# Kernel tuning notes

Measured on AMD Instinct MI355X. Metric: run time of the kernel, lower is better.

Reference implementation:

```python
import jax, jax.numpy as jnp
import numpy as np
import math

B, L, C, D, H, NLAYERS, DFF = 256, 100, 55, 512, 8, 3, 64


def _pos_embedding(length, d_model):
    pos = np.arange(length, dtype=np.float32)[:, None]
    div = np.exp(np.arange(0, d_model, 2, dtype=np.float32) * (-math.log(10000.0) / d_model))
    pe = np.zeros((length, d_model), dtype=np.float32)
    pe[:, 0::2] = np.sin(pos * div)
    pe[:, 1::2] = np.cos(pos * div)
    return jnp.asarray(pe)


def setup_inputs() -> dict:
    key = jax.random.key(0)
    ks = jax.random.split(key, 12)
    r = lambda k, s, sc: jax.random.normal(k, s, dtype=jnp.float32) * sc
    sD = 1.0 / math.sqrt(D)
    return {
        'x': r(ks[0], (B, L, C), 1.0),
        'tok_w': r(ks[1], (D, C, 3), 1.0 / math.sqrt(3 * C)),  # Conv1d(c_in->d_model, k=3, circular, no bias)
        'pe': _pos_embedding(L, D),
        'Wq': r(ks[2], (NLAYERS, D, D), sD), 'bq': jnp.zeros((NLAYERS, D), jnp.float32),
        'Wk': r(ks[3], (NLAYERS, D, D), sD), 'bk': jnp.zeros((NLAYERS, D), jnp.float32),
        'Wv': r(ks[4], (NLAYERS, D, D), sD), 'bv': jnp.zeros((NLAYERS, D), jnp.float32),
        'Wsig': r(ks[5], (NLAYERS, H, D), sD), 'bsig': jnp.zeros((NLAYERS, H), jnp.float32),
        'Wo': r(ks[6], (NLAYERS, D, D), sD), 'bo': jnp.zeros((NLAYERS, D), jnp.float32),
        'W1': r(ks[7], (NLAYERS, DFF, D), sD), 'b1': jnp.zeros((NLAYERS, DFF), jnp.float32),  # conv1 (1x1)
        'W2': r(ks[8], (NLAYERS, D, DFF), 1.0 / math.sqrt(DFF)), 'b2': jnp.zeros((NLAYERS, D), jnp.float32),  # conv2 (1x1)
        'proj_w': r(ks[9], (C, D), sD), 'proj_b': jnp.zeros((C,), jnp.float32),
    }


def _forward(x, tok_w, pe, Wq, bq, Wk, bk, Wv, bv, Wsig, bsig, Wo, bo, W1, b1, W2, b2, proj_w, proj_b):
    Bx, Lx, _ = x.shape
    nlayers, nH = Wsig.shape[0], Wsig.shape[1]
    d_model = Wq.shape[1]
    dk = d_model // nH
    scale = 1.0 / math.sqrt(dk)
    # token embedding: circular-padded Conv1d(k=3, no bias), then + positional embedding
    xc = jnp.pad(jnp.swapaxes(x, 1, 2), ((0, 0), (0, 0), (1, 1)), mode='wrap')  # [B,C,L+2]
    emb = jax.lax.conv_general_dilated(xc, tok_w, (1,), 'VALID', dimension_numbers=('NCW', 'OIW', 'NCW'))
    h = jnp.swapaxes(emb, 1, 2) + pe[None]  # [B,L,D]
    dist = jnp.abs(jnp.arange(Lx)[:, None] - jnp.arange(Lx)[None, :]).astype(h.dtype)  # |i-j|
    for l in range(nlayers):
        q = h @ Wq[l].T + bq[l]                       # [B,L,D]
        k = (h @ Wk[l].T + bk[l]).reshape(Bx, Lx, nH, dk)
        v = (h @ Wv[l].T + bv[l]).reshape(Bx, Lx, nH, dk)
        # NOTE: source applies sigma projection to the *projected* queries
        sigma = q @ Wsig[l].T + bsig[l]               # [B,L,H]
        qh = q.reshape(Bx, Lx, nH, dk)
        scores = jnp.einsum('blhe,bshe->bhls', qh, k)  # [B,H,L,L]
        series = jax.nn.softmax(scale * scores, axis=-1)
        # Gaussian prior branch (mask_flag=False; computed in source forward,
        # does not feed the module's returned output)
        sg = jnp.swapaxes(sigma, 1, 2)                 # [B,H,L]
        sg = jnp.power(3.0, jax.nn.sigmoid(sg * 5.0) + 1e-5) - 1.0
        sgE = sg[..., None]                            # [B,H,L,1]
        _prior = jnp.exp(-(dist ** 2)[None, None] / (2.0 * sgE ** 2)) / (math.sqrt(2.0 * math.pi) * sgE)
        o = jnp.einsum('bhls,bshd->blhd', series, v).reshape(Bx, Lx, d_model)
        h = h + (o @ Wo[l].T + bo[l])                  # residual 1 (dropout=identity at eval)
        y = jax.nn.gelu(h @ W1[l].T + b1[l], approximate=False)  # conv1 1x1 + gelu
        h = h + (y @ W2[l].T + b2[l])                  # conv2 1x1, residual 2
    return h @ proj_w.T + proj_b                       # [B,L,c_out]


def reference(x, tok_w, pe, Wq, bq, Wk, bk, Wv, bv, Wsig, bsig, Wo, bo, W1, b1, W2, b2, proj_w, proj_b):
    return _forward(x, tok_w, pe, Wq, bq, Wk, bk, Wv, bv, Wsig, bsig, Wo, bo, W1, b1, W2, b2, proj_w, proj_b)
```

## Files before the change

kernel.cpp:

```cpp
#include <hip/hip_runtime.h>
#include <stdint.h>

typedef unsigned short u16;
typedef __attribute__((ext_vector_type(8))) short short8;
typedef __attribute__((ext_vector_type(4))) float f32x4;

#define DEVI __device__ __forceinline__

#define BB   256
#define LL   100
#define CC   55
#define DD   512
#define HH   8
#define DKK  64
#define MM   (BB * LL)
#define KEMB 192
#define NSEG 17

DEVI float bf2f(u16 s) { union { unsigned int u; float f; } x; x.u = ((unsigned int)s) << 16; return x.f; }
DEVI u16 f2bf(float f) {
  union { float f; unsigned int u; } x; x.f = f;
  unsigned int u = x.u;
  return (u16)((u + 0x7FFFu + ((u >> 16) & 1u)) >> 16);
}

DEVI void async_lds16(const u16* gp, u16* lp) {
  __builtin_amdgcn_global_load_lds((const __attribute__((address_space(1))) void*)gp,
                                   (__attribute__((address_space(3))) void*)lp, 16, 0, 0);
}

DEVI void wave_lds_fence() {
  asm volatile("s_waitcnt lgkmcnt(0)" ::: "memory");
  __builtin_amdgcn_wave_barrier();
}

DEVI int swz_row(int r) { return (r & 3) ^ ((r >> 2) & 3); }

__global__ void detect_dtype(const u16* __restrict__ x, int* __restrict__ flag) {
  __shared__ int cnt[256];
  int tid = threadIdx.x;
  u16 u = x[2 * tid];
  int e = (u >> 7) & 0xFF;
  cnt[tid] = (e >= 0x5F && e <= 0x90) ? 1 : 0;
  __syncthreads();
  for (int s = 128; s > 0; s >>= 1) { if (tid < s) cnt[tid] += cnt[tid + s]; __syncthreads(); }
  if (tid == 0) *flag = (cnt[0] >= 160) ? 0 : 1;
}

struct Segs { const void* src[NSEG]; int off[NSEG + 1]; };

__global__ void convert_all(Segs s, const int* __restrict__ flag, u16* __restrict__ dst) {
  int i = blockIdx.x * 256 + threadIdx.x;
  if (i >= s.off[NSEG]) return;
  int sidx = 0;
#pragma unroll
  for (int k = 1; k < NSEG; k++) if (i >= s.off[k]) sidx = k;
  int j = i - s.off[sidx];
  u16 v;
  if (*flag) v = f2bf(((const float*)s.src[sidx])[j]);
  else       v = ((const u16*)s.src[sidx])[j];
  dst[i] = v;
}

__global__ void repack_w(const u16* __restrict__ tokw, u16* __restrict__ Wg) {
  int idx = blockIdx.x * 256 + threadIdx.x;
  if (idx >= 512 * KEMB) return;
  int d = idx / KEMB, j = idx % KEMB, k = j >> 6, c = j & 63;
  Wg[idx] = (c < CC) ? tokw[d * (CC * 3) + c * 3 + k] : (u16)0;
}

__global__ void repack_x(const u16* __restrict__ x, u16* __restrict__ Xg) {
  int idx = blockIdx.x * 256 + threadIdx.x;
  if (idx >= MM * KEMB) return;
  int m = idx / KEMB, j = idx % KEMB, k = j >> 6, c = j & 63;
  int b = m / LL, l = m % LL;
  int l2 = l + k - 1; l2 = (l2 + LL) % LL;
  Xg[idx] = (c < CC) ? x[(size_t)(b * LL + l2) * CC + c] : (u16)0;
}

struct GemmW { const u16* W[3]; const u16* bias[3]; void* out[3]; };

template<int BM, int BN, int NTT, int TAG, bool QKV, bool DIRECT>
__global__ __launch_bounds__(256)
void gemm_bt(const u16* __restrict__ A, int K, GemmW w,
             const u16* __restrict__ pe,
             const u16* __restrict__ resid,
             int dogelu,
             int ldo, int nvalid,
             const int* __restrict__ dtf)
{
  constexpr int BK = 32;
  constexpr int MI = BM / 32;
  constexpr int CW = BN / 2, NT = CW / 16;
  constexpr int SW = CW + 4;
  constexpr int STAGE_U16 = (BM + BN) * BK * 2;
  __shared__ alignas(16) u16 smem[STAGE_U16];
  u16* As = smem;
  u16* Bs = smem + BM * BK * 2;

  const int tid = threadIdx.x;
  const int lane = tid & 63;
  const int wv = __builtin_amdgcn_readfirstlane(tid >> 6);
  const int wm = wv & 1, wn = wv >> 1;
  const int l15 = lane & 15, qd = lane >> 4;
  const int swz = swz_row(l15);

  const int id = blockIdx.x;
  const int mpx = gridDim.x / (NTT * 8);
  const int xcd = id & 7, slot = id >> 3;
  const int m_t = xcd * mpx + slot / NTT;
  const int n_t = slot % NTT;
  const int m0 = m_t * BM;
  int n0 = n_t * BN;
  int sel = 0, n0l = n0;
  if (QKV) { sel = n0 >> 9; n0l = n0 & 511; }
  const u16* W = w.W[sel];
  const u16* bias = w.bias[sel];
  void* outp = w.out[sel];

  const f32x4 zf = {0.f, 0.f, 0.f, 0.f};
  f32x4 acc[MI][NT];
#pragma unroll
  for (int i = 0; i < MI; i++)
#pragma unroll
    for (int j = 0; j < NT; j++) acc[i][j] = zf;

  for (int k0 = 0; k0 < K; k0 += 2 * BK) {
    __syncthreads();
#pragma unroll
    for (int p = 0; p < 2; p++) {
      u16* Asp = As + p * BM * BK;
      u16* Bsp = Bs + p * BN * BK;
      const int kp = k0 + p * BK;
#pragma unroll
      for (int i = 0; i < BM / 64; i++) {
        int base = i * 256 + wv * 64;
        int idx = base + lane;
        int row = idx >> 2;
        int cs = ((idx & 3) ^ swz_row(row)) * 8;
        async_lds16(A + (size_t)(m0 + row) * K + kp + cs, Asp + base * 8);
      }
#pragma unroll
      for (int i = 0; i < BN / 64; i++) {
        int base = i * 256 + wv * 64;
        int idx = base + lane;
        int row = idx >> 2;
        int cs = ((idx & 3) ^ swz_row(row)) * 8;
        int gr = n0l + row; if (gr >= nvalid) gr = nvalid - 1;
        async_lds16(W + (size_t)gr * K + kp + cs, Bsp + base * 8);
      }
    }
    __syncthreads();

#pragma unroll
    for (int p = 0; p < 2; p++) {
      const u16* Asp = As + p * BM * BK;
      const u16* Bsp = Bs + p * BN * BK;
      short8 af[MI], bfr[NT];
#pragma unroll
      for (int mi = 0; mi < MI; mi++)
        af[mi] = *(const short8*)&Asp[(wm * (BM / 2) + mi * 16 + l15) * BK + ((qd ^ swz) * 8)];
#pragma unroll
      for (int ni = 0; ni < NT; ni++)
        bfr[ni] = *(const short8*)&Bsp[(wn * CW + ni * 16 + l15) * BK + ((qd ^ swz) * 8)];
#pragma unroll
      for (int mi = 0; mi < MI; mi++)
#pragma unroll
        for (int ni = 0; ni < NT; ni++)
          acc[mi][ni] = __builtin_amdgcn_mfma_f32_16x16x32_bf16(af[mi], bfr[ni], acc[mi][ni], 0, 0, 0);
    }
  }

  if (DIRECT) {
    const int sf = (dtf != nullptr) ? *dtf : 0;
#pragma unroll
    for (int mi = 0; mi < MI; mi++)
#pragma unroll
      for (int ni = 0; ni < NT; ni++) {
        int gcol = n0l + wn * CW + ni * 16 + l15;
        float bv = (bias && gcol < nvalid) ? bf2f(bias[gcol]) : 0.f;
#pragma unroll
        for (int r = 0; r < 4; r++) {
          int grow = m0 + wm * (BM / 2) + mi * 16 + qd * 4 + r;
          if (gcol < nvalid) {
            float v = acc[mi][ni][r] + bv;
            if (sf) ((float*)outp)[(size_t)grow * ldo + gcol] = v;
            else    ((u16*)outp)[(size_t)grow * ldo + gcol] = f2bf(v);
          }
        }
      }
    return;
  }

  __syncthreads();
  u16* slab = smem + wv * 16 * SW;
#pragma unroll
  for (int mi = 0; mi < MI; mi++) {
    const int lr = wm * (BM / 2) + mi * 16 + qd * 4;
    float v[NT][4];
    if (!QKV && resid) {
#pragma unroll
      for (int ni = 0; ni < NT; ni++) {
        int col = n0l + wn * CW + ni * 16 + l15;
#pragma unroll
        for (int r = 0; r < 4; r++)
          v[ni][r] = bf2f(resid[(size_t)(m0 + lr + r) * DD + col]);
      }
    } else {
#pragma unroll
      for (int ni = 0; ni < NT; ni++)
#pragma unroll
        for (int r = 0; r < 4; r++) v[ni][r] = 0.f;
    }
#pragma unroll
    for (int ni = 0; ni < NT; ni++) {
      const int lc = wn * CW + ni * 16 + l15;
      float bv = bias ? bf2f(bias[n0l + lc]) : 0.f;
#pragma unroll
      for (int r = 0; r < 4; r++) {
        float x = v[ni][r] + acc[mi][ni][r] + bv;
        if (!QKV && pe) x += bf2f(pe[((m0 + lr + r) % LL) * DD + n0l + lc]);
        if (!QKV && dogelu) x = 0.5f * x * (1.f + erff(x * 0.70710678118654752f));
        v[ni][r] = x;
      }
    }
#pragma unroll
    for (int ni = 0; ni < NT; ni++)
#pragma unroll
      for (int r = 0; r < 4; r++)
        slab[(qd * 4 + r) * SW + ni * 16 + l15] = f2bf(v[ni][r]);
    wave_lds_fence();
    if (BN == 128) {
      int r2 = lane >> 2, c2 = (lane & 3) * 16;
      int grow = m0 + wm * (BM / 2) + mi * 16 + r2;
      u16* op = (u16*)outp + (size_t)grow * ldo + n0l + wn * CW + c2;
      *(short8*)&op[0] = *(const short8*)&slab[r2 * SW + c2];
      *(short8*)&op[8] = *(const short8*)&slab[r2 * SW + c2 + 8];
    } else {
      if (lane < 32) {
        int r2 = lane >> 1, c2 = (lane & 1) * 16;
        int grow = m0 + wm * (BM / 2) + mi * 16 + r2;
        u16* op = (u16*)outp + (size_t)grow * ldo + n0l + wn * CW + c2;
        *(short8*)&op[0] = *(const short8*)&slab[r2 * SW + c2];
        *(short8*)&op[8] = *(const short8*)&slab[r2 * SW + c2 + 8];
      }
    }
    wave_lds_fence();
  }
}

__global__ __launch_bounds__(256)
void ffn_fused(const u16* __restrict__ h, const u16* __restrict__ W1,
               const u16* __restrict__ b1, const u16* __restrict__ W2,
               const u16* __restrict__ b2, u16* __restrict__ hout)
{
  constexpr int BM = 64, BK = 32, SW = 36;
  __shared__ alignas(16) u16 smem[4096 + 10496];
  u16* y      = smem;
  u16* shared = smem + 4096;
  u16* As  = shared;
  u16* Bs  = shared + 4096;
  u16* Bs2 = shared;
  u16* slabs = shared + 8192;

  const int tid = threadIdx.x;
  const int lane = tid & 63;
  const int wv = __builtin_amdgcn_readfirstlane(tid >> 6);
  const int wm = wv & 1, wn = wv >> 1;
  const int l15 = lane & 15, qd = lane >> 4;
  const int swz = swz_row(l15);
  const int id = blockIdx.x;
  const int mpx = gridDim.x >> 3;
  const int m0 = ((id & 7) * mpx + (id >> 3)) * BM;

  const int srow = tid >> 2;
  const int scs = ((tid & 3) ^ swz_row(srow)) * 8;
  const f32x4 zf = {0.f, 0.f, 0.f, 0.f};

  f32x4 acc[2][2];
#pragma unroll
  for (int i = 0; i < 2; i++)
#pragma unroll
    for (int j = 0; j < 2; j++) acc[i][j] = zf;

  for (int k0 = 0; k0 < DD; k0 += 64) {
    __syncthreads();
#pragma unroll
    for (int p = 0; p < 2; p++) {
      const int kp = k0 + p * BK;
      async_lds16(h  + (size_t)(m0 + srow) * DD + kp + scs, As + p * 2048 + tid * 8);
      async_lds16(W1 + (size_t)srow * DD + kp + scs,        Bs + p * 2048 + tid * 8);
    }
    __syncthreads();
#pragma unroll
    for (int p = 0; p < 2; p++) {
      short8 af[2], bfr[2];
#pragma unroll
      for (int mi = 0; mi < 2; mi++)
        af[mi] = *(const short8*)&As[p * 2048 + (wm * 32 + mi * 16 + l15) * BK + ((qd ^ swz) * 8)];
#pragma unroll
      for (int ni = 0; ni < 2; ni++)
        bfr[ni] = *(const short8*)&Bs[p * 2048 + (wn * 32 + ni * 16 + l15) * BK + ((qd ^ swz) * 8)];
#pragma unroll
      for (int mi = 0; mi < 2; mi++)
#pragma unroll
        for (int ni = 0; ni < 2; ni++)
          acc[mi][ni] = __builtin_amdgcn_mfma_f32_16x16x32_bf16(af[mi], bfr[ni], acc[mi][ni], 0, 0, 0);
    }
  }
#pragma unroll
  for (int mi = 0; mi < 2; mi++)
#pragma unroll
    for (int ni = 0; ni < 2; ni++) {
      float bv = bf2f(b1[wn * 32 + ni * 16 + l15]);
#pragma unroll
      for (int r = 0; r < 4; r++) {
        int row = wm * 32 + mi * 16 + qd * 4 + r;
        int kpos = ni * 16 + l15;
        int slot = ((kpos >> 3) ^ swz_row(row)) & 3;
        float x = acc[mi][ni][r] + bv;
        x = 0.5f * x * (1.f + erff(x * 0.70710678118654752f));
        y[wn * 2048 + row * BK + slot * 8 + (kpos & 7)] = f2bf(x);
      }
    }
  __syncthreads();

  auto stage2 = [&](int buf, int nc) {
#pragma unroll
    for (int p = 0; p < 2; p++)
      async_lds16(W2 + (size_t)(nc * 64 + srow) * 64 + p * BK + scs,
                  Bs2 + buf * 4096 + p * 2048 + tid * 8);
  };
  stage2(0, 0);
  int cur = 0;
  u16* slab = slabs + wv * 16 * SW;
  for (int nc = 0; nc < 8; nc++) {
    __syncthreads();
    if (nc + 1 < 8) stage2(cur ^ 1, nc + 1);
    f32x4 a2[2][2];
#pragma unroll
    for (int i = 0; i < 2; i++)
#pragma unroll
      for (int j = 0; j < 2; j++) a2[i][j] = zf;
#pragma unroll
    for (int p = 0; p < 2; p++) {
      short8 af[2], bfr[2];
#pragma unroll
      for (int mi = 0; mi < 2; mi++)
        af[mi] = *(const short8*)&y[p * 2048 + (wm * 32 + mi * 16 + l15) * BK + ((qd ^ swz) * 8)];
#pragma unroll
      for (int ni = 0; ni < 2; ni++)
        bfr[ni] = *(const short8*)&Bs2[cur * 4096 + p * 2048 + (wn * 32 + ni * 16 + l15) * BK + ((qd ^ swz) * 8)];
#pragma unroll
      for (int mi = 0; mi < 2; mi++)
#pragma unroll
        for (int ni = 0; ni < 2; ni++)
          a2[mi][ni] = __builtin_amdgcn_mfma_f32_16x16x32_bf16(af[mi], bfr[ni], a2[mi][ni], 0, 0, 0);
    }
    const int n0l = nc * 64;
#pragma unroll
    for (int mi = 0; mi < 2; mi++) {
      const int lr = wm * 32 + mi * 16 + qd * 4;
      float v[2][4];
#pragma unroll
      for (int ni = 0; ni < 2; ni++) {
        int col = n0l + wn * 32 + ni * 16 + l15;
        float bv = bf2f(b2[col]);
#pragma unroll
        for (int r = 0; r < 4; r++)
          v[ni][r] = bf2f(h[(size_t)(m0 + lr + r) * DD + col]) + a2[mi][ni][r] + bv;
      }
#pragma unroll
      for (int ni = 0; ni < 2; ni++)
#pragma unroll
        for (int r = 0; r < 4; r++)
          slab[(qd * 4 + r) * SW + ni * 16 + l15] = f2bf(v[ni][r]);
      wave_lds_fence();
      if (lane < 32) {
        int r2 = lane >> 1, c2 = (lane & 1) * 16;
        int grow = m0 + wm * 32 + mi * 16 + r2;
        u16* op = hout + (size_t)grow * DD + n0l + wn * 32 + c2;
        *(short8*)&op[0] = *(const short8*)&slab[r2 * SW + c2];
        *(short8*)&op[8] = *(const short8*)&slab[r2 * SW + c2 + 8];
      }
      wave_lds_fence();
    }
    cur ^= 1;
  }
}

__global__ __launch_bounds__(256)
void attn(const u16* __restrict__ qg, const u16* __restrict__ kg,
          const u16* __restrict__ vg, u16* __restrict__ og)
{
  constexpr int LP = 128;
  __shared__ alignas(16) u16 Ks[LP * DKK];
  __shared__ alignas(16) u16 Vt[DKK * LP];
  __shared__ alignas(16) u16 Ps[LP * LP];

  const int bh = blockIdx.x;
  const int b = bh >> 3, h = bh & 7;
  const size_t base = (size_t)b * LL * DD + (size_t)h * DKK;
  const int tid = threadIdx.x, lane = tid & 63, wv = tid >> 6;
  const int l15 = lane & 15, qd = lane >> 4;
  const short8 z8 = {0, 0, 0, 0, 0, 0, 0, 0};

  for (int i = tid; i < LP * 8; i += 256) {
    int row = i >> 3, e8 = (i & 7) * 8;
    short8 val = z8;
    if (row < LL) val = *(const short8*)(kg + base + (size_t)row * DD + e8);
    *(short8*)&Ks[row * DKK + e8] = val;
  }
  for (int i = tid; i < LP * 8; i += 256) {
    int j = i & 127, d0 = (i >> 7) * 8;
    short8 val = z8;
    if (j < LL) val = *(const short8*)(vg + base + (size_t)j * DD + d0);
#pragma unroll
    for (int u = 0; u < 8; u++) Vt[(d0 + u) * LP + j] = (u16)val[u];
  }
  __syncthreads();

  const f32x4 zf = {0.f, 0.f, 0.f, 0.f};
  f32x4 sc[2][8];
#pragma unroll
  for (int it = 0; it < 2; it++)
#pragma unroll
    for (int jt = 0; jt < 8; jt++) sc[it][jt] = zf;

  short8 af[2][2];
#pragma unroll
  for (int it = 0; it < 2; it++) {
    int row = (2 * wv + it) * 16 + l15;
#pragma unroll
    for (int ks = 0; ks < 2; ks++) {
      short8 val = z8;
      if (row < LL) val = *(const short8*)(qg + base + (size_t)row * DD + ks * 32 + qd * 8);
      af[it][ks] = val;
    }
  }
#pragma unroll
  for (int jt = 0; jt < 8; jt++) {
    short8 b0 = *(const short8*)&Ks[(jt * 16 + l15) * DKK + qd * 8];
    short8 b1 = *(const short8*)&Ks[(jt * 16 + l15) * DKK + 32 + qd * 8];
#pragma unroll
    for (int it = 0; it < 2; it++) {
      sc[it][jt] = __builtin_amdgcn_mfma_f32_16x16x32_bf16(af[it][0], b0, sc[it][jt], 0, 0, 0);
      sc[it][jt] = __builtin_amdgcn_mfma_f32_16x16x32_bf16(af[it][1], b1, sc[it][jt], 0, 0, 0);
    }
  }

  constexpr float scale = 0.125f;
#pragma unroll
  for (int it = 0; it < 2; it++) {
    int rb = (2 * wv + it) * 16 + qd * 4;
#pragma unroll
    for (int r = 0; r < 4; r++) {
      float vals[8];
      float mx = -1e30f;
#pragma unroll
      for (int jt = 0; jt < 8; jt++) {
        int col = jt * 16 + l15;
        float vv = sc[it][jt][r] * scale;
        if (col >= LL) vv = -1e30f;
        vals[jt] = vv;
        mx = fmaxf(mx, vv);
      }
#pragma unroll
      for (int off = 1; off < 16; off <<= 1) mx = fmaxf(mx, __shfl_xor(mx, off, 64));
      float s = 0.f;
#pragma unroll
      for (int jt = 0; jt < 8; jt++) { float p = __expf(vals[jt] - mx); vals[jt] = p; s += p; }
#pragma unroll
      for (int off = 1; off < 16; off <<= 1) s += __shfl_xor(s, off, 64);
      float inv = 1.f / s;
      int rowp = rb + r;
#pragma unroll
      for (int jt = 0; jt < 8; jt++) Ps[rowp * LP + jt * 16 + l15] = f2bf(vals[jt] * inv);
    }
  }
  __syncthreads();

  f32x4 oc[2][4];
#pragma unroll
  for (int it = 0; it < 2; it++)
#pragma unroll
    for (int dt = 0; dt < 4; dt++) oc[it][dt] = zf;
#pragma unroll
  for (int ks = 0; ks < 4; ks++) {
    short8 ap[2];
#pragma unroll
    for (int it = 0; it < 2; it++)
      ap[it] = *(const short8*)&Ps[((2 * wv + it) * 16 + l15) * LP + ks * 32 + qd * 8];
#pragma unroll
    for (int dt = 0; dt < 4; dt++) {
      short8 bv = *(const short8*)&Vt[(dt * 16 + l15) * LP + ks * 32 + qd * 8];
#pragma unroll
      for (int it = 0; it < 2; it++)
        oc[it][dt] = __builtin_amdgcn_mfma_f32_16x16x32_bf16(ap[it], bv, oc[it][dt], 0, 0, 0);
    }
  }

  __syncthreads();
  u16* Os = Ps;
#pragma unroll
  for (int it = 0; it < 2; it++) {
    int rb = (2 * wv + it) * 16 + qd * 4;
#pragma unroll
    for (int dt = 0; dt < 4; dt++)
#pragma unroll
      for (int r = 0; r < 4; r++)
        Os[(rb + r) * DKK + dt * 16 + l15] = f2bf(oc[it][dt][r]);
  }
  __syncthreads();
  {
    int row = tid >> 1, c0 = (tid & 1) * 32;
    if (row < LL) {
      u16* op = og + base + (size_t)row * DD + c0;
#pragma unroll
      for (int c = 0; c < 32; c += 8)
        *(short8*)&op[c] = *(const short8*)&Os[row * DKK + c0 + c];
    }
  }
}

extern "C" void kernel_launch(void* const* d_in, const int* in_sizes, int n_in,
                              void* d_out, int out_size, void* d_ws, size_t ws_size,
                              hipStream_t stream)
{
  (void)in_sizes; (void)n_in; (void)out_size; (void)ws_size;

  char* ws = (char*)d_ws;
  size_t off = 0;
  auto alloc = [&](size_t bytes) { char* p = ws + off; off += (bytes + 255) & ~(size_t)255; return p; };
  int* dflag = (int*)alloc(256);
  static const int seg_sizes[NSEG] = {
    MM * CC, DD * CC * 3, LL * DD,
    3 * DD * DD, 3 * DD, 3 * DD * DD, 3 * DD, 3 * DD * DD, 3 * DD,
    3 * DD * DD, 3 * DD, 3 * 64 * DD, 3 * 64, 3 * DD * 64, 3 * DD,
    CC * DD, CC
  };
  static const int seg_input[NSEG] = {0, 1, 2, 3, 4, 5, 6, 7, 8, 11, 12, 13, 14, 15, 16, 17, 18};
  int total = 0, segoff[NSEG + 1];
  for (int i = 0; i < NSEG; i++) { segoff[i] = total; total += seg_sizes[i]; }
  segoff[NSEG] = total;
  u16* canon = (u16*)alloc((size_t)total * 2);

  u16* hbf = (u16*)alloc((size_t)MM * DD * 2);
  u16* qb  = (u16*)alloc((size_t)MM * DD * 2);
  u16* kb  = (u16*)alloc((size_t)MM * DD * 2);
  u16* vb  = (u16*)alloc((size_t)MM * DD * 2);
  u16* ob  = (u16*)alloc((size_t)MM * DD * 2);
  u16* Wg  = (u16*)alloc((size_t)512 * KEMB * 2);
  u16* Xg  = qb;

  const u16* xc  = canon + segoff[0];
  const u16* twc = canon + segoff[1];
  const u16* pec = canon + segoff[2];
  const u16* Wqc = canon + segoff[3];  const u16* bqc = canon + segoff[4];
  const u16* Wkc = canon + segoff[5];  const u16* bkc = canon + segoff[6];
  const u16* Wvc = canon + segoff[7];  const u16* bvc = canon + segoff[8];
  const u16* Woc = canon + segoff[9];  const u16* boc = canon + segoff[10];
  const u16* W1c = canon + segoff[11]; const u16* b1c = canon + segoff[12];
  const u16* W2c = canon + segoff[13]; const u16* b2c = canon + segoff[14];
  const u16* pwc = canon + segoff[15]; const u16* pbc = canon + segoff[16];

  Segs sg;
  for (int i = 0; i < NSEG; i++) { sg.src[i] = d_in[seg_input[i]]; sg.off[i] = segoff[i]; }
  sg.off[NSEG] = total;

  dim3 blk(256);
  detect_dtype<<<dim3(1), blk, 0, stream>>>((const u16*)d_in[0], dflag);
  convert_all<<<dim3((total + 255) / 256), blk, 0, stream>>>(sg, dflag, canon);
  repack_w<<<dim3((512 * KEMB + 255) / 256), blk, 0, stream>>>(twc, Wg);
  repack_x<<<dim3((MM * KEMB + 255) / 256), blk, 0, stream>>>(xc, Xg);

  auto W1of = [&](const u16* p) { GemmW g{}; g.W[0] = g.W[1] = g.W[2] = p; return g; };

  { GemmW g = W1of(Wg); g.out[0] = hbf;
    gemm_bt<128, 64, 8, 0, false, false><<<dim3(1600), blk, 0, stream>>>(Xg, KEMB, g, pec, nullptr, 0, DD, DD, nullptr); }

  for (int l = 0; l < 3; l++) {
    const u16* Wq_l = Wqc + (size_t)l * DD * DD; const u16* bq_l = bqc + l * DD;
    const u16* Wk_l = Wkc + (size_t)l * DD * DD; const u16* bk_l = bkc + l * DD;
    const u16* Wv_l = Wvc + (size_t)l * DD * DD; const u16* bv_l = bvc + l * DD;
    const u16* Wo_l = Woc + (size_t)l * DD * DD; const u16* bo_l = boc + l * DD;
    const u16* W1_l = W1c + (size_t)l * 64 * DD; const u16* b1_l = b1c + l * 64;
    const u16* W2_l = W2c + (size_t)l * DD * 64; const u16* b2_l = b2c + l * DD;

    { GemmW g{}; g.W[0] = Wq_l; g.W[1] = Wk_l; g.W[2] = Wv_l;
      g.bias[0] = bq_l; g.bias[1] = bk_l; g.bias[2] = bv_l;
      g.out[0] = qb; g.out[1] = kb; g.out[2] = vb;
      gemm_bt<128, 64, 24, 1, true, false><<<dim3(4800), blk, 0, stream>>>(hbf, DD, g, nullptr, nullptr, 0, DD, DD, nullptr); }

    attn<<<dim3(BB * HH), blk, 0, stream>>>(qb, kb, vb, ob);

    { GemmW g = W1of(Wo_l); g.bias[0] = g.bias[1] = g.bias[2] = bo_l; g.out[0] = g.out[1] = g.out[2] = hbf;
      gemm_bt<128, 64, 8, 2, false, false><<<dim3(1600), blk, 0, stream>>>(ob, DD, g, nullptr, hbf, 0, DD, DD, nullptr); }

    ffn_fused<<<dim3(400), blk, 0, stream>>>(hbf, W1_l, b1_l, W2_l, b2_l, hbf);
  }
  { GemmW g = W1of(pwc); g.bias[0] = pbc; g.out[0] = d_out;
    gemm_bt<64, 64, 1, 5, false, true><<<dim3(400), blk, 0, stream>>>(hbf, DD, g, nullptr, nullptr, 0, CC, CC, dflag); }
}
```

Before: 655.1 us.

## Split FFN output columns across two blocks and shrink attention LDS footprint

The fused FFN kernel now launches twice as many blocks, and each block handles half of the output column chunks. Both halves recompute the first GEMM plus GELU for the same rows, so the FFN writes into a ping-pong h buffer to avoid an in-place read/write race. The attention kernel drops its 32KB probability buffer: probabilities stay in registers and are written in two halves into the reused K buffer, which cuts LDS use to raise occupancy. The cost is redundant W1 compute in the FFN and extra barriers in attention.

Result: no change. 648.0 us (-1.1%).

```diff
diff --git a/kernel.cpp b/kernel.cpp
--- a/kernel.cpp
+++ b/kernel.cpp
@@ -271,7 +271,9 @@
   const int swz = swz_row(l15);
   const int id = blockIdx.x;
   const int mpx = gridDim.x >> 3;
-  const int m0 = ((id & 7) * mpx + (id >> 3)) * BM;
+  const int lid = (id & 7) * mpx + (id >> 3);
+  const int m0 = (lid >> 1) * BM;
+  const int nh = lid & 1;
 
   const int srow = tid >> 2;
   const int scs = ((tid & 3) ^ swz_row(srow)) * 8;
@@ -331,12 +333,13 @@
       async_lds16(W2 + (size_t)(nc * 64 + srow) * 64 + p * BK + scs,
                   Bs2 + buf * 4096 + p * 2048 + tid * 8);
   };
-  stage2(0, 0);
+  const int nc0 = nh * 4, nc1 = nc0 + 4;
+  stage2(0, nc0);
   int cur = 0;
   u16* slab = slabs + wv * 16 * SW;
-  for (int nc = 0; nc < 8; nc++) {
+  for (int nc = nc0; nc < nc1; nc++) {
     __syncthreads();
-    if (nc + 1 < 8) stage2(cur ^ 1, nc + 1);
+    if (nc + 1 < nc1) stage2(cur ^ 1, nc + 1);
     f32x4 a2[2][2];
 #pragma unroll
     for (int i = 0; i < 2; i++)
@@ -396,7 +399,6 @@
   constexpr int LP = 128;
   __shared__ alignas(16) u16 Ks[LP * DKK];
   __shared__ alignas(16) u16 Vt[DKK * LP];
-  __shared__ alignas(16) u16 Ps[LP * LP];
 
   const int bh = blockIdx.x;
   const int b = bh >> 3, h = bh & 7;
@@ -452,7 +454,6 @@
   constexpr float scale = 0.125f;
 #pragma unroll
   for (int it = 0; it < 2; it++) {
-    int rb = (2 * wv + it) * 16 + qd * 4;
 #pragma unroll
     for (int r = 0; r < 4; r++) {
       float vals[8];
@@ -473,24 +474,35 @@
 #pragma unroll
       for (int off = 1; off < 16; off <<= 1) s += __shfl_xor(s, off, 64);
       float inv = 1.f / s;
-      int rowp = rb + r;
-#pragma unroll
-      for (int jt = 0; jt < 8; jt++) Ps[rowp * LP + jt * 16 + l15] = f2bf(vals[jt] * inv);
-    }
-  }
-  __syncthreads();
-
+#pragma unroll
+      for (int jt = 0; jt < 8; jt++) sc[it][jt][r] = vals[jt] * inv;
+    }
+  }
+  __syncthreads();
+
+  u16* Pc = Ks;
   f32x4 oc[2][4];
 #pragma unroll
   for (int it = 0; it < 2; it++)
 #pragma unroll
     for (int dt = 0; dt < 4; dt++) oc[it][dt] = zf;
-#pragma unroll
-  for (int ks = 0; ks < 4; ks++) {
+
+#pragma unroll
+  for (int it = 0; it < 2; it++) {
+    int rb = (2 * wv + it) * 16 + qd * 4;
+#pragma unroll
+    for (int r = 0; r < 4; r++)
+#pragma unroll
+      for (int jt = 0; jt < 4; jt++)
+        Pc[(rb + r) * DKK + jt * 16 + l15] = f2bf(sc[it][jt][r]);
+  }
+  __syncthreads();
+#pragma unroll
+  for (int ks = 0; ks < 2; ks++) {
     short8 ap[2];
 #pragma unroll
     for (int it = 0; it < 2; it++)
-      ap[it] = *(const short8*)&Ps[((2 * wv + it) * 16 + l15) * LP + ks * 32 + qd * 8];
+      ap[it] = *(const short8*)&Pc[((2 * wv + it) * 16 + l15) * DKK + ks * 32 + qd * 8];
 #pragma unroll
     for (int dt = 0; dt < 4; dt++) {
       short8 bv = *(const short8*)&Vt[(dt * 16 + l15) * LP + ks * 32 + qd * 8];
@@ -499,9 +511,35 @@
         oc[it][dt] = __builtin_amdgcn_mfma_f32_16x16x32_bf16(ap[it], bv, oc[it][dt], 0, 0, 0);
     }
   }
-
-  __syncthreads();
-  u16* Os = Ps;
+  __syncthreads();
+
+#pragma unroll
+  for (int it = 0; it < 2; it++) {
+    int rb = (2 * wv + it) * 16 + qd * 4;
+#pragma unroll
+    for (int r = 0; r < 4; r++)
+#pragma unroll
+      for (int jt = 4; jt < 8; jt++)
+        Pc[(rb + r) * DKK + (jt - 4) * 16 + l15] = f2bf(sc[it][jt][r]);
+  }
+  __syncthreads();
+#pragma unroll
+  for (int ks = 2; ks < 4; ks++) {
+    short8 ap[2];
+#pragma unroll
+    for (int it = 0; it < 2; it++)
+      ap[it] = *(const short8*)&Pc[((2 * wv + it) * 16 + l15) * DKK + (ks - 2) * 32 + qd * 8];
+#pragma unroll
+    for (int dt = 0; dt < 4; dt++) {
+      short8 bv = *(const short8*)&Vt[(dt * 16 + l15) * LP + ks * 32 + qd * 8];
+#pragma unroll
+      for (int it = 0; it < 2; it++)
+        oc[it][dt] = __builtin_amdgcn_mfma_f32_16x16x32_bf16(ap[it], bv, oc[it][dt], 0, 0, 0);
+    }
+  }
+
+  __syncthreads();
+  u16* Os = Ks;
 #pragma unroll
   for (int it = 0; it < 2; it++) {
     int rb = (2 * wv + it) * 16 + qd * 4;
@@ -546,6 +584,7 @@
   u16* canon = (u16*)alloc((size_t)total * 2);
 
   u16* hbf = (u16*)alloc((size_t)MM * DD * 2);
+  u16* h2  = (u16*)alloc((size_t)MM * DD * 2);
   u16* qb  = (u16*)alloc((size_t)MM * DD * 2);
   u16* kb  = (u16*)alloc((size_t)MM * DD * 2);
   u16* vb  = (u16*)alloc((size_t)MM * DD * 2);
@@ -579,6 +618,7 @@
   { GemmW g = W1of(Wg); g.out[0] = hbf;
     gemm_bt<128, 64, 8, 0, false, false><<<dim3(1600), blk, 0, stream>>>(Xg, KEMB, g, pec, nullptr, 0, DD, DD, nullptr); }
 
+  u16* hc = hbf;
   for (int l = 0; l < 3; l++) {
     const u16* Wq_l = Wqc + (size_t)l * DD * DD; const u16* bq_l = bqc + l * DD;
     const u16* Wk_l = Wkc + (size_t)l * DD * DD; const u16* bk_l = bkc + l * DD;
@@ -590,15 +630,17 @@
     { GemmW g{}; g.W[0] = Wq_l; g.W[1] = Wk_l; g.W[2] = Wv_l;
       g.bias[0] = bq_l; g.bias[1] = bk_l; g.bias[2] = bv_l;
       g.out[0] = qb; g.out[1] = kb; g.out[2] = vb;
-      gemm_bt<128, 64, 24, 1, true, false><<<dim3(4800), blk, 0, stream>>>(hbf, DD, g, nullptr, nullptr, 0, DD, DD, nullptr); }
+      gemm_bt<128, 64, 24, 1, true, false><<<dim3(4800), blk, 0, stream>>>(hc, DD, g, nullptr, nullptr, 0, DD, DD, nullptr); }
 
     attn<<<dim3(BB * HH), blk, 0, stream>>>(qb, kb, vb, ob);
 
-    { GemmW g = W1of(Wo_l); g.bias[0] = g.bias[1] = g.bias[2] = bo_l; g.out[0] = g.out[1] = g.out[2] = hbf;
-      gemm_bt<128, 64, 8, 2, false, false><<<dim3(1600), blk, 0, stream>>>(ob, DD, g, nullptr, hbf, 0, DD, DD, nullptr); }
-
-    ffn_fused<<<dim3(400), blk, 0, stream>>>(hbf, W1_l, b1_l, W2_l, b2_l, hbf);
+    { GemmW g = W1of(Wo_l); g.bias[0] = g.bias[1] = g.bias[2] = bo_l; g.out[0] = g.out[1] = g.out[2] = hc;
+      gemm_bt<128, 64, 8, 2, false, false><<<dim3(1600), blk, 0, stream>>>(ob, DD, g, nullptr, hc, 0, DD, DD, nullptr); }
+
+    u16* hn = (hc == hbf) ? h2 : hbf;
+    ffn_fused<<<dim3(800), blk, 0, stream>>>(hc, W1_l, b1_l, W2_l, b2_l, hn);
+    hc = hn;
   }
   { GemmW g = W1of(pwc); g.bias[0] = pbc; g.out[0] = d_out;
-    gemm_bt<64, 64, 1, 5, false, true><<<dim3(400), blk, 0, stream>>>(hbf, DD, g, nullptr, nullptr, 0, CC, CC, dflag); }
-}
+    gemm_bt<64, 64, 1, 5, false, true><<<dim3(400), blk, 0, stream>>>(hc, DD, g, nullptr, nullptr, 0, CC, CC, dflag); }
+}
```
